# Kernel tuning notes

Hardware: AMD Instinct MI355X
Metric: run time of the kernel (lower is better)

## Reference

```python
import jax, jax.numpy as jnp
import numpy as np


def setup_inputs() -> dict:
    key = jax.random.key(0)
    k1, k2 = jax.random.split(key)
    B, S, H = 8, 2048, 1024
    lstm_output = jax.random.normal(k1, (B, S, H), dtype=jnp.float32)
    # xavier-uniform-like init for the bilinear weight
    limit = float(np.sqrt(6.0 / (H + H)))
    attention_weights = jax.random.uniform(k2, (H, H), dtype=jnp.float32, minval=-limit, maxval=limit)
    return {"lstm_output": lstm_output, "attention_weights": attention_weights}


def reference(lstm_output, attention_weights):
    # scores[b,i,j] = (x[b,i] @ W) . x[b,j]
    xw = jnp.einsum('bsh,hk->bsk', lstm_output, attention_weights)      # [B,S,H]
    scores = jnp.einsum('bsk,btk->bst', xw, lstm_output)                # [B,S,S]
    attn = jax.nn.softmax(scores, axis=-1)                              # [B,S,S]
    context = jnp.einsum('bst,bth->bsh', attn, lstm_output)             # [B,S,H]
    return (context, attn)
```

## Files before the change

kernel.cpp:

```cpp
#include <hip/hip_runtime.h>
#include <hip/hip_bf16.h>


#define BB 8
#define SS 2048
#define HH 1024

typedef __attribute__((ext_vector_type(8))) short bf16x8;
typedef __attribute__((ext_vector_type(4))) float f32x4;

__device__ __forceinline__ void async_load16(const void* gsrc, void* ldst) {
    typedef const unsigned int __attribute__((address_space(1)))* gp_t;
    typedef unsigned int __attribute__((address_space(3)))* lp_t;
    __builtin_amdgcn_global_load_lds((gp_t)gsrc, (lp_t)ldst, 16, 0, 0);
}

__device__ __forceinline__ unsigned short f2b(float f) {
    __hip_bfloat16 h = __float2bfloat16(f);
    return *(unsigned short*)&h;
}
__device__ __forceinline__ float b2f(unsigned short u) {
    __hip_bfloat16 h = *(__hip_bfloat16*)&u;
    return __bfloat162float(h);
}

__global__ __launch_bounds__(256) void split_x(const float* __restrict__ X,
                                               unsigned short* __restrict__ Xh,
                                               unsigned short* __restrict__ Xl) {
    const size_t i = ((size_t)blockIdx.x * 256 + threadIdx.x) * 8;
    float4 a = *(const float4*)(X + i);
    float4 b = *(const float4*)(X + i + 4);
    ushort4 h0, h1, l0, l1;
    float v, hf;
    v = a.x; h0.x = f2b(v); hf = b2f(h0.x); l0.x = f2b(v - hf);
    v = a.y; h0.y = f2b(v); hf = b2f(h0.y); l0.y = f2b(v - hf);
    v = a.z; h0.z = f2b(v); hf = b2f(h0.z); l0.z = f2b(v - hf);
    v = a.w; h0.w = f2b(v); hf = b2f(h0.w); l0.w = f2b(v - hf);
    v = b.x; h1.x = f2b(v); hf = b2f(h1.x); l1.x = f2b(v - hf);
    v = b.y; h1.y = f2b(v); hf = b2f(h1.y); l1.y = f2b(v - hf);
    v = b.z; h1.z = f2b(v); hf = b2f(h1.z); l1.z = f2b(v - hf);
    v = b.w; h1.w = f2b(v); hf = b2f(h1.w); l1.w = f2b(v - hf);
    *(ushort4*)(Xh + i) = h0; *(ushort4*)(Xh + i + 4) = h1;
    *(ushort4*)(Xl + i) = l0; *(ushort4*)(Xl + i + 4) = l1;
}

__global__ __launch_bounds__(256) void split_wT(const float* __restrict__ W,
                                                unsigned short* __restrict__ Th,
                                                unsigned short* __restrict__ Tl) {
    const int k0 = blockIdx.y * 64, n0 = blockIdx.x * 64;
    __shared__ float tile[64][65];
#pragma unroll
    for (int q = 0; q < 16; q++) {
        int idx = q * 256 + threadIdx.x;
        int r = idx >> 6, c = idx & 63;
        tile[r][c] = W[(size_t)(k0 + r) * HH + n0 + c];
    }
    __syncthreads();
#pragma unroll
    for (int q = 0; q < 16; q++) {
        int idx = q * 256 + threadIdx.x;
        int r = idx >> 6, c = idx & 63;
        float v = tile[c][r];
        unsigned short h = f2b(v);
        Th[(size_t)(n0 + r) * HH + k0 + c] = h;
        Tl[(size_t)(n0 + r) * HH + k0 + c] = f2b(v - b2f(h));
    }
}

__global__ __launch_bounds__(256) void gemm_xw3(const unsigned short* __restrict__ Ah,
                                                const unsigned short* __restrict__ Al,
                                                const unsigned short* __restrict__ Bh,
                                                const unsigned short* __restrict__ Bl,
                                                unsigned short* __restrict__ Ch,
                                                unsigned short* __restrict__ Cl) {
    const int b = blockIdx.z;
    const int i0 = blockIdx.y * 128, n0 = blockIdx.x * 128;
    const unsigned short* A_h = Ah + (size_t)b * SS * HH;
    const unsigned short* A_l = Al + (size_t)b * SS * HH;

    __shared__ __align__(16) unsigned short AsH[128 * 32];
    __shared__ __align__(16) unsigned short AsL[128 * 32];
    __shared__ __align__(16) unsigned short BsH[128 * 32];
    __shared__ __align__(16) unsigned short BsL[128 * 32];

    const int tid = threadIdx.x;
    const int wave = tid >> 6, lane = tid & 63;
    const int m16 = lane & 15, quad = lane >> 4;
    const int wy = wave >> 1, wx = wave & 1;
    const int rowA = tid >> 2;
    const int kq = (tid & 3) ^ ((rowA >> 1) & 3);

    f32x4 acc[4][4] = {};

    for (int k0 = 0; k0 < HH; k0 += 32) {
        const size_t ga0 = (size_t)(i0 + rowA) * HH + k0 + kq * 8;
        const size_t ga1 = (size_t)(i0 + 64 + rowA) * HH + k0 + kq * 8;
        const size_t gb0 = (size_t)(n0 + rowA) * HH + k0 + kq * 8;
        const size_t gb1 = (size_t)(n0 + 64 + rowA) * HH + k0 + kq * 8;
        async_load16(A_h + ga0, (char*)AsH + wave * 1024);
        async_load16(A_h + ga1, (char*)AsH + 4096 + wave * 1024);
        async_load16(A_l + ga0, (char*)AsL + wave * 1024);
        async_load16(A_l + ga1, (char*)AsL + 4096 + wave * 1024);
        async_load16(Bh + gb0, (char*)BsH + wave * 1024);
        async_load16(Bh + gb1, (char*)BsH + 4096 + wave * 1024);
        async_load16(Bl + gb0, (char*)BsL + wave * 1024);
        async_load16(Bl + gb1, (char*)BsL + 4096 + wave * 1024);
        __syncthreads();

        const int cs = quad ^ ((m16 >> 1) & 3);
        const int offA = (wy * 64 + m16) * 32 + cs * 8;
        const int offB = (wx * 64 + m16) * 32 + cs * 8;
        bf16x8 ah[4], al[4], bh[4], bl[4];
#pragma unroll
        for (int r = 0; r < 4; r++) {
            ah[r] = *(const bf16x8*)(AsH + offA + r * 16 * 32);
            al[r] = *(const bf16x8*)(AsL + offA + r * 16 * 32);
        }
#pragma unroll
        for (int c = 0; c < 4; c++) {
            bh[c] = *(const bf16x8*)(BsH + offB + c * 16 * 32);
            bl[c] = *(const bf16x8*)(BsL + offB + c * 16 * 32);
        }
#pragma unroll
        for (int r = 0; r < 4; r++)
#pragma unroll
            for (int c = 0; c < 4; c++) {
                acc[r][c] = __builtin_amdgcn_mfma_f32_16x16x32_bf16(ah[r], bh[c], acc[r][c], 0, 0, 0);
                acc[r][c] = __builtin_amdgcn_mfma_f32_16x16x32_bf16(ah[r], bl[c], acc[r][c], 0, 0, 0);
                acc[r][c] = __builtin_amdgcn_mfma_f32_16x16x32_bf16(al[r], bh[c], acc[r][c], 0, 0, 0);
            }
        __syncthreads();
    }

    unsigned short* ChB = Ch + (size_t)b * SS * HH;
    unsigned short* ClB = Cl + (size_t)b * SS * HH;
#pragma unroll
    for (int r = 0; r < 4; r++) {
        const int row = i0 + wy * 64 + r * 16 + quad * 4;
#pragma unroll
        for (int c = 0; c < 4; c++) {
            const int col = n0 + wx * 64 + c * 16 + m16;
#pragma unroll
            for (int reg = 0; reg < 4; reg++) {
                float v = acc[r][c][reg];
                unsigned short h = f2b(v);
                ChB[(size_t)(row + reg) * HH + col] = h;
                ClB[(size_t)(row + reg) * HH + col] = f2b(v - b2f(h));
            }
        }
    }
}

__global__ __launch_bounds__(256) void gemm_sc3(const unsigned short* __restrict__ Ah,
                                                const unsigned short* __restrict__ Al,
                                                const unsigned short* __restrict__ Bh,
                                                const unsigned short* __restrict__ Bl,
                                                float* __restrict__ SC) {
    const int b = blockIdx.z;
    const int i0 = blockIdx.y * 128, j0 = blockIdx.x * 128;
    const unsigned short* A_h = Ah + (size_t)b * SS * HH;
    const unsigned short* A_l = Al + (size_t)b * SS * HH;
    const unsigned short* B_h = Bh + (size_t)b * SS * HH;
    const unsigned short* B_l = Bl + (size_t)b * SS * HH;

    __shared__ __align__(16) unsigned short AsH[128 * 32];
    __shared__ __align__(16) unsigned short AsL[128 * 32];
    __shared__ __align__(16) unsigned short BsH[128 * 32];
    __shared__ __align__(16) unsigned short BsL[128 * 32];

    const int tid = threadIdx.x;
    const int wave = tid >> 6, lane = tid & 63;
    const int m16 = lane & 15, quad = lane >> 4;
    const int wy = wave >> 1, wx = wave & 1;
    const int rowA = tid >> 2;
    const int kq = (tid & 3) ^ ((rowA >> 1) & 3);

    f32x4 acc[4][4] = {};

    for (int k0 = 0; k0 < HH; k0 += 32) {
        const size_t ga0 = (size_t)(i0 + rowA) * HH + k0 + kq * 8;
        const size_t ga1 = (size_t)(i0 + 64 + rowA) * HH + k0 + kq * 8;
        const size_t gb0 = (size_t)(j0 + rowA) * HH + k0 + kq * 8;
        const size_t gb1 = (size_t)(j0 + 64 + rowA) * HH + k0 + kq * 8;
        async_load16(A_h + ga0, (char*)AsH + wave * 1024);
        async_load16(A_h + ga1, (char*)AsH + 4096 + wave * 1024);
        async_load16(A_l + ga0, (char*)AsL + wave * 1024);
        async_load16(A_l + ga1, (char*)AsL + 4096 + wave * 1024);
        async_load16(B_h + gb0, (char*)BsH + wave * 1024);
        async_load16(B_h + gb1, (char*)BsH + 4096 + wave * 1024);
        async_load16(B_l + gb0, (char*)BsL + wave * 1024);
        async_load16(B_l + gb1, (char*)BsL + 4096 + wave * 1024);
        __syncthreads();

        const int cs = quad ^ ((m16 >> 1) & 3);
        const int offA = (wy * 64 + m16) * 32 + cs * 8;
        const int offB = (wx * 64 + m16) * 32 + cs * 8;
        bf16x8 ah[4], al[4], bh[4], bl[4];
#pragma unroll
        for (int r = 0; r < 4; r++) {
            ah[r] = *(const bf16x8*)(AsH + offA + r * 16 * 32);
            al[r] = *(const bf16x8*)(AsL + offA + r * 16 * 32);
        }
#pragma unroll
        for (int c = 0; c < 4; c++) {
            bh[c] = *(const bf16x8*)(BsH + offB + c * 16 * 32);
            bl[c] = *(const bf16x8*)(BsL + offB + c * 16 * 32);
        }
#pragma unroll
        for (int r = 0; r < 4; r++)
#pragma unroll
            for (int c = 0; c < 4; c++) {
                acc[r][c] = __builtin_amdgcn_mfma_f32_16x16x32_bf16(ah[r], bh[c], acc[r][c], 0, 0, 0);
                acc[r][c] = __builtin_amdgcn_mfma_f32_16x16x32_bf16(ah[r], bl[c], acc[r][c], 0, 0, 0);
                acc[r][c] = __builtin_amdgcn_mfma_f32_16x16x32_bf16(al[r], bh[c], acc[r][c], 0, 0, 0);
            }
        __syncthreads();
    }

    float* Cb = SC + (size_t)b * SS * SS;
#pragma unroll
    for (int r = 0; r < 4; r++) {
        const int row = i0 + wy * 64 + r * 16 + quad * 4;
#pragma unroll
        for (int c = 0; c < 4; c++) {
            const int col = j0 + wx * 64 + c * 16 + m16;
#pragma unroll
            for (int reg = 0; reg < 4; reg++)
                Cb[(size_t)(row + reg) * SS + col] = acc[r][c][reg];
        }
    }
}

__global__ __launch_bounds__(256) void softmax_rows(float* __restrict__ P,
                                                    unsigned short* __restrict__ Pb) {
    const size_t row = blockIdx.x;
    float4* p4 = (float4*)(P + row * SS);
    const int tid = threadIdx.x;
    float4 v0 = p4[tid], v1 = p4[tid + 256];
    float m = fmaxf(fmaxf(fmaxf(v0.x, v0.y), fmaxf(v0.z, v0.w)),
                    fmaxf(fmaxf(v1.x, v1.y), fmaxf(v1.z, v1.w)));
#pragma unroll
    for (int off = 32; off; off >>= 1) m = fmaxf(m, __shfl_xor(m, off));
    __shared__ float red[4];
    const int wid = tid >> 6, lane = tid & 63;
    if (lane == 0) red[wid] = m;
    __syncthreads();
    m = fmaxf(fmaxf(red[0], red[1]), fmaxf(red[2], red[3]));
    v0.x = __expf(v0.x - m); v0.y = __expf(v0.y - m);
    v0.z = __expf(v0.z - m); v0.w = __expf(v0.w - m);
    v1.x = __expf(v1.x - m); v1.y = __expf(v1.y - m);
    v1.z = __expf(v1.z - m); v1.w = __expf(v1.w - m);
    float s = v0.x + v0.y + v0.z + v0.w + v1.x + v1.y + v1.z + v1.w;
#pragma unroll
    for (int off = 32; off; off >>= 1) s += __shfl_xor(s, off);
    __syncthreads();
    if (lane == 0) red[wid] = s;
    __syncthreads();
    s = red[0] + red[1] + red[2] + red[3];
    const float inv = 1.0f / s;
    v0.x *= inv; v0.y *= inv; v0.z *= inv; v0.w *= inv;
    v1.x *= inv; v1.y *= inv; v1.z *= inv; v1.w *= inv;
    p4[tid] = v0;
    p4[tid + 256] = v1;
    ushort4* b4 = (ushort4*)(Pb + row * SS);
    ushort4 u0 = { f2b(v0.x), f2b(v0.y), f2b(v0.z), f2b(v0.w) };
    ushort4 u1 = { f2b(v1.x), f2b(v1.y), f2b(v1.z), f2b(v1.w) };
    b4[tid] = u0;
    b4[tid + 256] = u1;
}

__global__ __launch_bounds__(256) void transpose_cvt(const float* __restrict__ X,
                                                     unsigned short* __restrict__ XT) {
    const int b = blockIdx.z;
    const int t0 = blockIdx.y * 64;
    const int h0 = blockIdx.x * 64;
    __shared__ float tile[64][65];
    const float* Xb = X + (size_t)b * SS * HH;
    unsigned short* Tb = XT + (size_t)b * HH * SS;
#pragma unroll
    for (int q = 0; q < 16; q++) {
        int idx = q * 256 + threadIdx.x;
        int r = idx >> 6, c = idx & 63;
        tile[r][c] = Xb[(size_t)(t0 + r) * HH + h0 + c];
    }
    __syncthreads();
#pragma unroll
    for (int q = 0; q < 16; q++) {
        int idx = q * 256 + threadIdx.x;
        int r = idx >> 6, c = idx & 63;
        Tb[(size_t)(h0 + r) * SS + t0 + c] = f2b(tile[c][r]);
    }
}

__global__ __launch_bounds__(256) void gemm_ctx_mfma(const unsigned short* __restrict__ Ab,
                                                     const unsigned short* __restrict__ Bt,
                                                     float* __restrict__ C) {
    const int b = blockIdx.z;
    const int i0 = blockIdx.y * 128;
    const int n0 = blockIdx.x * 128;
    const unsigned short* A = Ab + (size_t)b * SS * SS;
    const unsigned short* B = Bt + (size_t)b * HH * SS;

    __shared__ __align__(16) unsigned short As[128 * 32];
    __shared__ __align__(16) unsigned short Bs[128 * 32];

    const int tid = threadIdx.x;
    const int wave = tid >> 6, lane = tid & 63;
    const int m16 = lane & 15, quad = lane >> 4;
    const int wy = wave >> 1, wx = wave & 1;
    const int rowA = tid >> 2;
    const int kq = (tid & 3) ^ ((rowA >> 1) & 3);

    f32x4 acc[4][4] = {};

    for (int k0 = 0; k0 < SS; k0 += 32) {
        async_load16(A + (size_t)(i0 + rowA) * SS + k0 + kq * 8, (char*)As + wave * 1024);
        async_load16(A + (size_t)(i0 + 64 + rowA) * SS + k0 + kq * 8, (char*)As + 4096 + wave * 1024);
        async_load16(B + (size_t)(n0 + rowA) * SS + k0 + kq * 8, (char*)Bs + wave * 1024);
        async_load16(B + (size_t)(n0 + 64 + rowA) * SS + k0 + kq * 8, (char*)Bs + 4096 + wave * 1024);
        __syncthreads();

        const int cs = quad ^ ((m16 >> 1) & 3);
        const unsigned short* pA = As + (wy * 64 + m16) * 32 + cs * 8;
        const unsigned short* pB = Bs + (wx * 64 + m16) * 32 + cs * 8;
        bf16x8 af[4], bfr[4];
#pragma unroll
        for (int r = 0; r < 4; r++) af[r] = *(const bf16x8*)(pA + r * 16 * 32);
#pragma unroll
        for (int c = 0; c < 4; c++) bfr[c] = *(const bf16x8*)(pB + c * 16 * 32);
#pragma unroll
        for (int r = 0; r < 4; r++)
#pragma unroll
            for (int c = 0; c < 4; c++)
                acc[r][c] = __builtin_amdgcn_mfma_f32_16x16x32_bf16(af[r], bfr[c], acc[r][c], 0, 0, 0);
        __syncthreads();
    }

    float* Cb = C + (size_t)b * SS * HH;
#pragma unroll
    for (int r = 0; r < 4; r++) {
        const int row = i0 + wy * 64 + r * 16 + quad * 4;
#pragma unroll
        for (int c = 0; c < 4; c++) {
            const int col = n0 + wx * 64 + c * 16 + m16;
#pragma unroll
            for (int reg = 0; reg < 4; reg++)
                Cb[(size_t)(row + reg) * HH + col] = acc[r][c][reg];
        }
    }
}

extern "C" void kernel_launch(void* const* d_in, const int* in_sizes, int n_in,
                              void* d_out, int out_size, void* d_ws, size_t ws_size,
                              hipStream_t stream) {
    const float* X = (const float*)d_in[0];
    const float* W = (const float*)d_in[1];
    float* ctx  = (float*)d_out;
    float* attn = ctx + (size_t)BB * SS * HH;

    char* ws = (char*)d_ws;
    unsigned short* x_hi  = (unsigned short*)ws;
    unsigned short* x_lo  = (unsigned short*)(ws + ((size_t)32 << 20));
    unsigned short* wt_hi = (unsigned short*)(ws + ((size_t)64 << 20));
    unsigned short* wt_lo = (unsigned short*)(ws + ((size_t)66 << 20));
    unsigned short* xT     = x_hi;
    unsigned short* attn_b = x_lo;

    unsigned short* xw_hi = (unsigned short*)d_out;
    unsigned short* xw_lo = xw_hi + (size_t)BB * SS * HH;

    dim3 blk(256);
    split_x <<<dim3(BB * SS * HH / (8 * 256)), blk, 0, stream>>>(X, x_hi, x_lo);
    split_wT<<<dim3(HH / 64, HH / 64), blk, 0, stream>>>(W, wt_hi, wt_lo);
    gemm_xw3<<<dim3(HH / 128, SS / 128, BB), blk, 0, stream>>>(x_hi, x_lo, wt_hi, wt_lo, xw_hi, xw_lo);
    gemm_sc3<<<dim3(SS / 128, SS / 128, BB), blk, 0, stream>>>(xw_hi, xw_lo, x_hi, x_lo, attn);
    transpose_cvt<<<dim3(HH / 64, SS / 64, BB), blk, 0, stream>>>(X, xT);
    softmax_rows <<<dim3(BB * SS), blk, 0, stream>>>(attn, attn_b);
    gemm_ctx_mfma<<<dim3(HH / 128, SS / 128, BB), blk, 0, stream>>>(attn_b, xT, ctx);
}
```

Before: 724.6 us.

## Rewrite score GEMM as 256x256 eight-wave double-buffered pipelined kernel

The split-bf16 score GEMM moves from 128x128 tiles with 4 waves and a load-sync-compute loop to 256x256 tiles with 8 waves. Its 128KB of LDS is double-buffered, async global-to-LDS loads for the next k-step are interleaved with four MFMA phases, and s_setprio raises MFMA priority. The goal is to hide memory latency and raise data reuse per tile. In exchange it needs hand-tuned vmcnt waits and barriers that could be fragile, and the larger tiles mean fewer blocks and less occupancy per CU.

```diff
diff --git a/kernel.cpp b/kernel.cpp
--- a/kernel.cpp
+++ b/kernel.cpp
@@ -151,84 +151,133 @@
     }
 }
 
-__global__ __launch_bounds__(256) void gemm_sc3(const unsigned short* __restrict__ Ah,
-                                                const unsigned short* __restrict__ Al,
-                                                const unsigned short* __restrict__ Bh,
-                                                const unsigned short* __restrict__ Bl,
-                                                float* __restrict__ SC) {
+__global__ __launch_bounds__(512, 2) void gemm_sc3_8p(const unsigned short* __restrict__ Ah,
+                                                      const unsigned short* __restrict__ Al,
+                                                      const unsigned short* __restrict__ Bh,
+                                                      const unsigned short* __restrict__ Bl,
+                                                      float* __restrict__ SC) {
     const int b = blockIdx.z;
-    const int i0 = blockIdx.y * 128, j0 = blockIdx.x * 128;
+    const int i0 = blockIdx.y * 256, j0 = blockIdx.x * 256;
     const unsigned short* A_h = Ah + (size_t)b * SS * HH;
     const unsigned short* A_l = Al + (size_t)b * SS * HH;
     const unsigned short* B_h = Bh + (size_t)b * SS * HH;
     const unsigned short* B_l = Bl + (size_t)b * SS * HH;
 
-    __shared__ __align__(16) unsigned short AsH[128 * 32];
-    __shared__ __align__(16) unsigned short AsL[128 * 32];
-    __shared__ __align__(16) unsigned short BsH[128 * 32];
-    __shared__ __align__(16) unsigned short BsL[128 * 32];
+    __shared__ __align__(16) unsigned short lds[65536];
 
     const int tid = threadIdx.x;
     const int wave = tid >> 6, lane = tid & 63;
     const int m16 = lane & 15, quad = lane >> 4;
-    const int wy = wave >> 1, wx = wave & 1;
-    const int rowA = tid >> 2;
-    const int kq = (tid & 3) ^ ((rowA >> 1) & 3);
-
-    f32x4 acc[4][4] = {};
-
-    for (int k0 = 0; k0 < HH; k0 += 32) {
-        const size_t ga0 = (size_t)(i0 + rowA) * HH + k0 + kq * 8;
-        const size_t ga1 = (size_t)(i0 + 64 + rowA) * HH + k0 + kq * 8;
-        const size_t gb0 = (size_t)(j0 + rowA) * HH + k0 + kq * 8;
-        const size_t gb1 = (size_t)(j0 + 64 + rowA) * HH + k0 + kq * 8;
-        async_load16(A_h + ga0, (char*)AsH + wave * 1024);
-        async_load16(A_h + ga1, (char*)AsH + 4096 + wave * 1024);
-        async_load16(A_l + ga0, (char*)AsL + wave * 1024);
-        async_load16(A_l + ga1, (char*)AsL + 4096 + wave * 1024);
-        async_load16(B_h + gb0, (char*)BsH + wave * 1024);
-        async_load16(B_h + gb1, (char*)BsH + 4096 + wave * 1024);
-        async_load16(B_l + gb0, (char*)BsL + wave * 1024);
-        async_load16(B_l + gb1, (char*)BsL + 4096 + wave * 1024);
-        __syncthreads();
-
-        const int cs = quad ^ ((m16 >> 1) & 3);
-        const int offA = (wy * 64 + m16) * 32 + cs * 8;
-        const int offB = (wx * 64 + m16) * 32 + cs * 8;
-        bf16x8 ah[4], al[4], bh[4], bl[4];
-#pragma unroll
-        for (int r = 0; r < 4; r++) {
-            ah[r] = *(const bf16x8*)(AsH + offA + r * 16 * 32);
-            al[r] = *(const bf16x8*)(AsL + offA + r * 16 * 32);
-        }
-#pragma unroll
-        for (int c = 0; c < 4; c++) {
-            bh[c] = *(const bf16x8*)(BsH + offB + c * 16 * 32);
-            bl[c] = *(const bf16x8*)(BsL + offB + c * 16 * 32);
-        }
-#pragma unroll
-        for (int r = 0; r < 4; r++)
-#pragma unroll
-            for (int c = 0; c < 4; c++) {
-                acc[r][c] = __builtin_amdgcn_mfma_f32_16x16x32_bf16(ah[r], bh[c], acc[r][c], 0, 0, 0);
-                acc[r][c] = __builtin_amdgcn_mfma_f32_16x16x32_bf16(ah[r], bl[c], acc[r][c], 0, 0, 0);
-                acc[r][c] = __builtin_amdgcn_mfma_f32_16x16x32_bf16(al[r], bh[c], acc[r][c], 0, 0, 0);
-            }
-        __syncthreads();
+    const int wy = wave >> 2, wx = wave & 3;
+    const int rP = tid >> 2;
+    const int kq = (tid & 3) ^ ((rP >> 1) & 3);
+    const int cs = quad ^ ((m16 >> 1) & 3);
+    const int wt16 = wave * 1024;
+    const int rowA_off = (rP & 63) + ((rP >> 6) << 7);
+    const int rowB_off = ((rP >> 5) << 6) + (rP & 31);
+
+    const size_t aOff = (size_t)(i0 + rowA_off) * HH + kq * 8;
+    const size_t bOff = (size_t)(j0 + rowB_off) * HH + kq * 8;
+
+    f32x4 acc[2][4][2][2] = {};
+    bf16x8 a_h[4], a_l[4], b_h[2][2], b_l[2][2];
+
+#define STG_A(mh, kt, buf) do { \
+        const size_t o_ = aOff + (size_t)(mh) * 64 * HH + (size_t)(kt) * 32; \
+        async_load16(A_h + o_, (char*)lds + ((buf) * 32768 + (mh) * 4096) * 2 + wt16); \
+        async_load16(A_l + o_, (char*)lds + ((buf) * 32768 + 8192 + (mh) * 4096) * 2 + wt16); \
+    } while (0)
+#define STG_B(nh, kt, buf) do { \
+        const size_t o_ = bOff + (size_t)(nh) * 32 * HH + (size_t)(kt) * 32; \
+        async_load16(B_h + o_, (char*)lds + ((buf) * 32768 + 16384 + (nh) * 4096) * 2 + wt16); \
+        async_load16(B_l + o_, (char*)lds + ((buf) * 32768 + 24576 + (nh) * 4096) * 2 + wt16); \
+    } while (0)
+#define RD_A(mh, buf) do { \
+        const int s0_ = (buf) * 32768 + ((mh) * 128 + wy * 64 + m16) * 32 + cs * 8; \
+        _Pragma("unroll") for (int mi = 0; mi < 4; ++mi) { \
+            a_h[mi] = *(const bf16x8*)&lds[s0_ + mi * 512]; \
+            a_l[mi] = *(const bf16x8*)&lds[8192 + s0_ + mi * 512]; \
+        } } while (0)
+#define RD_B(nh, buf) do { \
+        const int s0_ = (buf) * 32768 + ((nh) * 128 + wx * 32 + m16) * 32 + cs * 8; \
+        _Pragma("unroll") for (int nj = 0; nj < 2; ++nj) { \
+            b_h[nh][nj] = *(const bf16x8*)&lds[16384 + s0_ + nj * 512]; \
+            b_l[nh][nj] = *(const bf16x8*)&lds[24576 + s0_ + nj * 512]; \
+        } } while (0)
+#define MFMA_PH(mh, nh) \
+        __builtin_amdgcn_s_setprio(1); \
+        _Pragma("unroll") for (int mi = 0; mi < 4; ++mi) \
+        _Pragma("unroll") for (int nj = 0; nj < 2; ++nj) { \
+            acc[mh][mi][nh][nj] = __builtin_amdgcn_mfma_f32_16x16x32_bf16(a_h[mi], b_h[nh][nj], acc[mh][mi][nh][nj], 0, 0, 0); \
+            acc[mh][mi][nh][nj] = __builtin_amdgcn_mfma_f32_16x16x32_bf16(a_h[mi], b_l[nh][nj], acc[mh][mi][nh][nj], 0, 0, 0); \
+            acc[mh][mi][nh][nj] = __builtin_amdgcn_mfma_f32_16x16x32_bf16(a_l[mi], b_h[nh][nj], acc[mh][mi][nh][nj], 0, 0, 0); \
+        } \
+        __builtin_amdgcn_s_setprio(0);
+
+    STG_A(0, 0, 0); STG_A(1, 0, 0);
+    STG_B(0, 0, 0); STG_B(1, 0, 0);
+    STG_B(0, 1, 1); STG_B(1, 1, 1);
+    asm volatile("s_waitcnt vmcnt(4)" ::: "memory");
+    __builtin_amdgcn_s_barrier();
+    RD_B(0, 0); RD_B(1, 0);
+
+    for (int kt = 0; kt < 32; ++kt) {
+        const int bufc = kt & 1, bufn = bufc ^ 1;
+        const int ktA = kt < 31 ? kt + 1 : 31;
+        const int ktB = kt < 30 ? kt + 2 : 31;
+        RD_A(0, bufc);
+        STG_A(0, ktA, bufn);
+        __builtin_amdgcn_s_barrier();
+        __builtin_amdgcn_sched_barrier(0);
+        MFMA_PH(0, 0)
+        __builtin_amdgcn_sched_barrier(0);
+        __builtin_amdgcn_s_barrier();
+        asm volatile("s_waitcnt vmcnt(6)" ::: "memory");
+        STG_A(1, ktA, bufn);
+        __builtin_amdgcn_s_barrier();
+        __builtin_amdgcn_sched_barrier(0);
+        MFMA_PH(0, 1)
+        __builtin_amdgcn_sched_barrier(0);
+        __builtin_amdgcn_s_barrier();
+        asm volatile("s_waitcnt vmcnt(6)" ::: "memory");
+        RD_A(1, bufc);
+        STG_B(0, ktB, bufc);
+        __builtin_amdgcn_s_barrier();
+        __builtin_amdgcn_sched_barrier(0);
+        MFMA_PH(1, 0)
+        __builtin_amdgcn_sched_barrier(0);
+        RD_B(0, bufn);
+        __builtin_amdgcn_s_barrier();
+        asm volatile("s_waitcnt vmcnt(4)" ::: "memory");
+        STG_B(1, ktB, bufc);
+        __builtin_amdgcn_s_barrier();
+        __builtin_amdgcn_sched_barrier(0);
+        MFMA_PH(1, 1)
+        __builtin_amdgcn_sched_barrier(0);
+        RD_B(1, bufn);
+        __builtin_amdgcn_s_barrier();
     }
 
     float* Cb = SC + (size_t)b * SS * SS;
 #pragma unroll
-    for (int r = 0; r < 4; r++) {
-        const int row = i0 + wy * 64 + r * 16 + quad * 4;
-#pragma unroll
-        for (int c = 0; c < 4; c++) {
-            const int col = j0 + wx * 64 + c * 16 + m16;
-#pragma unroll
-            for (int reg = 0; reg < 4; reg++)
-                Cb[(size_t)(row + reg) * SS + col] = acc[r][c][reg];
-        }
-    }
+    for (int mh = 0; mh < 2; ++mh)
+#pragma unroll
+        for (int mi = 0; mi < 4; ++mi)
+#pragma unroll
+            for (int nh = 0; nh < 2; ++nh)
+#pragma unroll
+                for (int nj = 0; nj < 2; ++nj) {
+                    const int row = i0 + wy * 128 + mh * 64 + mi * 16 + quad * 4;
+                    const int col = j0 + wx * 64 + nh * 32 + nj * 16 + m16;
+#pragma unroll
+                    for (int reg = 0; reg < 4; ++reg)
+                        Cb[(size_t)(row + reg) * SS + col] = acc[mh][mi][nh][nj][reg];
+                }
+#undef STG_A
+#undef STG_B
+#undef RD_A
+#undef RD_B
+#undef MFMA_PH
 }
 
 __global__ __launch_bounds__(256) void softmax_rows(float* __restrict__ P,
@@ -373,7 +422,7 @@
     split_x <<<dim3(BB * SS * HH / (8 * 256)), blk, 0, stream>>>(X, x_hi, x_lo);
     split_wT<<<dim3(HH / 64, HH / 64), blk, 0, stream>>>(W, wt_hi, wt_lo);
     gemm_xw3<<<dim3(HH / 128, SS / 128, BB), blk, 0, stream>>>(x_hi, x_lo, wt_hi, wt_lo, xw_hi, xw_lo);
-    gemm_sc3<<<dim3(SS / 128, SS / 128, BB), blk, 0, stream>>>(xw_hi, xw_lo, x_hi, x_lo, attn);
+    gemm_sc3_8p<<<dim3(SS / 256, SS / 256, BB), dim3(512), 0, stream>>>(xw_hi, xw_lo, x_hi, x_lo, attn);
     transpose_cvt<<<dim3(HH / 64, SS / 64, BB), blk, 0, stream>>>(X, xT);
     softmax_rows <<<dim3(BB * SS), blk, 0, stream>>>(attn, attn_b);
     gemm_ctx_mfma<<<dim3(HH / 128, SS / 128, BB), blk, 0, stream>>>(attn_b, xT, ctx);
```

Measured after the change: 679.8 us. 1.07x faster.
